# Kernel tuning notes

Measured on AMD Instinct MI355X. Metric: run time of the kernel, lower is better.

## Reference

```python
import jax, jax.numpy as jnp
import numpy as np


def pairwise_dist(x):
    # Euclidean cdist via the expansion trick; grad-safe sqrt (0 grad at 0, like torch).
    sq = jnp.sum(x * x, axis=1)
    d2 = sq[:, None] + sq[None, :] - 2.0 * (x @ x.T)
    d2 = jnp.maximum(d2, 0.0)
    pos = d2 > 0
    return jnp.where(pos, jnp.sqrt(jnp.where(pos, d2, 1.0)), 0.0)


def knn_mask(dist, k):
    # per-row ascending sort; skip index 0 (self), take next k neighbors
    idx = jnp.argsort(dist, axis=1)[:, 1:k + 1]            # [N, k]
    n = dist.shape[0]
    return jnp.zeros_like(dist).at[jnp.arange(n)[:, None], idx].set(1.0)


def setup_inputs() -> dict:
    key = jax.random.key(0)
    k1, k2 = jax.random.split(key)
    N, D, K = 8192, 64, 12
    latent = jax.random.normal(k1, (N, D), dtype=jnp.float32)
    latent_norm = jnp.ones((), dtype=jnp.float32)
    X = jax.random.normal(k2, (N, D), dtype=jnp.float32)
    dist_X = pairwise_dist(X)
    pair_mask_X = knn_mask(dist_X, K)
    return {"latent": latent, "latent_norm": latent_norm,
            "dist_X": dist_X, "pair_mask_X": pair_mask_X, "k": K}


def reference(latent, latent_norm, dist_X, pair_mask_X, k):
    n = latent.shape[0]
    dist_Z = pairwise_dist(latent) / latent_norm
    pair_mask_Z = knn_mask(dist_Z, k)

    mask_diff = pair_mask_Z - pair_mask_X
    matched = (n * k - jnp.sum(mask_diff != 0) * 0.5) / (n * k)

    # match_edges == 'symmetric'
    sig1 = dist_X * pair_mask_X
    sig1_2 = dist_Z * pair_mask_X
    distance1_2 = jnp.sum(jnp.square(sig1 - sig1_2))
    sig2 = dist_Z * pair_mask_Z
    sig2_1 = dist_X * pair_mask_Z
    distance2_1 = jnp.sum(jnp.square(sig2_1 - sig2))
    distance = distance1_2 + distance2_1
    return (distance, matched, distance1_2, distance2_1)
```

## Files before the change

### kernel.cpp

```cpp
#include <hip/hip_runtime.h>
#include <stdint.h>

constexpr int NPTS = 8192;
constexpr int DIM  = 64;
constexpr int KNN  = 12;

constexpr int RT = 64;
constexpr int CT = 64;
constexpr int CS = 4;
constexpr int STRIPE = NPTS / CS;
constexpr int NCHUNK = STRIPE / CT;
constexpr int LSTR = 72;

constexpr unsigned long long SENTINEL = 0xFFFFFFFFFFFFFFFFull;

typedef short bf16x8 __attribute__((ext_vector_type(8)));
typedef float f32x4  __attribute__((ext_vector_type(4)));

__device__ __forceinline__ unsigned short f2bf(float x) {
  unsigned u = __float_as_uint(x);
  return (unsigned short)((u + 0x7FFFu + ((u >> 16) & 1u)) >> 16);
}
__device__ __forceinline__ float bf2f(unsigned short h) {
  return __uint_as_float(((unsigned)h) << 16);
}

__global__ __launch_bounds__(256) void init_kernel(float* out, int* ecnt) {
  int g = blockIdx.x * 256 + threadIdx.x;
  if (g < NPTS) ecnt[g] = 0;
  if (g < 4) out[g] = 0.0f;
}

__global__ __launch_bounds__(256) void conv_kernel(
    const float* __restrict__ latent, unsigned short* __restrict__ Lh,
    unsigned short* __restrict__ Ll, float* __restrict__ sq) {
  int i = blockIdx.x * 256 + threadIdx.x;
  const float4* p = reinterpret_cast<const float4*>(latent + (size_t)i * DIM);
  float s = 0.f;
#pragma unroll
  for (int t = 0; t < DIM / 4; ++t) {
    float4 v = p[t];
    s += v.x * v.x + v.y * v.y + v.z * v.z + v.w * v.w;
    ushort4 h, l;
    h.x = f2bf(v.x); l.x = f2bf(v.x - bf2f(h.x));
    h.y = f2bf(v.y); l.y = f2bf(v.y - bf2f(h.y));
    h.z = f2bf(v.z); l.z = f2bf(v.z - bf2f(h.z));
    h.w = f2bf(v.w); l.w = f2bf(v.w - bf2f(h.w));
    *reinterpret_cast<ushort4*>(Lh + (size_t)i * DIM + t * 4) = h;
    *reinterpret_cast<ushort4*>(Ll + (size_t)i * DIM + t * 4) = l;
  }
  sq[i] = s;
}

__global__ __launch_bounds__(256) void scan_mask(
    const float* __restrict__ mask_X, const float* __restrict__ dist_X,
    int* __restrict__ ecnt, int* __restrict__ ecol, float* __restrict__ edx) {
  const int total4 = NPTS * NPTS / 4;
  int stride = gridDim.x * 256;
  for (int idx4 = blockIdx.x * 256 + threadIdx.x; idx4 < total4; idx4 += stride) {
    float4 m = reinterpret_cast<const float4*>(mask_X)[idx4];
    if (m.x == 0.f && m.y == 0.f && m.z == 0.f && m.w == 0.f) continue;
    int base = idx4 * 4;
    float mv[4] = {m.x, m.y, m.z, m.w};
#pragma unroll
    for (int c = 0; c < 4; ++c) {
      if (mv[c] != 0.f) {
        int pos = base + c;
        int i = pos >> 13, j = pos & (NPTS - 1);
        int slot = atomicAdd(&ecnt[i], 1);
        if (slot < KNN) {
          ecol[i * KNN + slot] = j;
          edx[i * KNN + slot] = dist_X[pos];
        }
      }
    }
  }
}

__device__ __forceinline__ void topk_insert(unsigned long long cand,
                                            unsigned long long pk[KNN]) {
#pragma unroll
  for (int s = KNN - 1; s >= 0; --s) {
    bool belongs = cand < pk[s];
    bool shift = (s > 0) && (cand < pk[s - 1]);
    unsigned long long nv = shift ? pk[s - 1] : cand;
    if (belongs) pk[s] = nv;
  }
}

__global__ __launch_bounds__(256, 2) void dz_main(
    const unsigned short* __restrict__ Lh, const unsigned short* __restrict__ Ll,
    const float* __restrict__ sq, unsigned long long* __restrict__ topk_ws) {
  __shared__ unsigned short Ah[RT * LSTR], Al[RT * LSTR];
  __shared__ unsigned short Bh[CT * LSTR], Bl[CT * LSTR];
  __shared__ unsigned long long buf[RT * CT];
  __shared__ int   cnt[RT];
  __shared__ float thr[RT];
  __shared__ float sqA[RT];
  __shared__ float sqB[CT];

  const int tid = threadIdx.x;
  const int tile = blockIdx.x / CS;
  const int split = blockIdx.x % CS;
  const int ib = tile * RT;
  const int jb0 = split * STRIPE;

  const int wid = tid >> 6;
  const int lane = tid & 63;
  const int quad = lane >> 4;
  const int l16 = lane & 15;
  const int wr = wid >> 1;
  const int wc = wid & 1;

#pragma unroll
  for (int it = 0; it < 2; ++it) {
    int f = it * 256 + tid;
    int r = f >> 3, c = f & 7;
    const uint4* sh = reinterpret_cast<const uint4*>(Lh + (size_t)(ib + r) * DIM + c * 8);
    const uint4* sl = reinterpret_cast<const uint4*>(Ll + (size_t)(ib + r) * DIM + c * 8);
    *reinterpret_cast<uint4*>(&Ah[r * LSTR + c * 8]) = *sh;
    *reinterpret_cast<uint4*>(&Al[r * LSTR + c * 8]) = *sl;
  }
  if (tid < RT) { sqA[tid] = sq[ib + tid]; thr[tid] = 3.4e38f; }

  unsigned long long pk[KNN];
#pragma unroll
  for (int t = 0; t < KNN; ++t) pk[t] = SENTINEL;

  for (int ch = 0; ch < NCHUNK; ++ch) {
    const int jb = jb0 + ch * CT;
    __syncthreads();
#pragma unroll
    for (int it = 0; it < 2; ++it) {
      int f = it * 256 + tid;
      int r = f >> 3, c = f & 7;
      const uint4* sh = reinterpret_cast<const uint4*>(Lh + (size_t)(jb + r) * DIM + c * 8);
      const uint4* sl = reinterpret_cast<const uint4*>(Ll + (size_t)(jb + r) * DIM + c * 8);
      *reinterpret_cast<uint4*>(&Bh[r * LSTR + c * 8]) = *sh;
      *reinterpret_cast<uint4*>(&Bl[r * LSTR + c * 8]) = *sl;
    }
    if (tid < CT) sqB[tid] = sq[jb + tid];
    if (tid < RT) cnt[tid] = 0;
    __syncthreads();

    f32x4 acc[2][2];
#pragma unroll
    for (int rb = 0; rb < 2; ++rb)
#pragma unroll
      for (int cb = 0; cb < 2; ++cb) acc[rb][cb] = (f32x4){0.f, 0.f, 0.f, 0.f};

#pragma unroll
    for (int kk = 0; kk < 2; ++kk) {
      const int ko = kk * 32 + quad * 8;
      bf16x8 ah[2], al[2], bh[2], bl[2];
#pragma unroll
      for (int rb = 0; rb < 2; ++rb) {
        int row = wr * 32 + rb * 16 + l16;
        ah[rb] = *reinterpret_cast<const bf16x8*>(&Ah[row * LSTR + ko]);
        al[rb] = *reinterpret_cast<const bf16x8*>(&Al[row * LSTR + ko]);
      }
#pragma unroll
      for (int cb = 0; cb < 2; ++cb) {
        int col = wc * 32 + cb * 16 + l16;
        bh[cb] = *reinterpret_cast<const bf16x8*>(&Bh[col * LSTR + ko]);
        bl[cb] = *reinterpret_cast<const bf16x8*>(&Bl[col * LSTR + ko]);
      }
#pragma unroll
      for (int rb = 0; rb < 2; ++rb)
#pragma unroll
        for (int cb = 0; cb < 2; ++cb) {
          acc[rb][cb] = __builtin_amdgcn_mfma_f32_16x16x32_bf16(ah[rb], bh[cb], acc[rb][cb], 0, 0, 0);
          acc[rb][cb] = __builtin_amdgcn_mfma_f32_16x16x32_bf16(ah[rb], bl[cb], acc[rb][cb], 0, 0, 0);
          acc[rb][cb] = __builtin_amdgcn_mfma_f32_16x16x32_bf16(al[rb], bh[cb], acc[rb][cb], 0, 0, 0);
        }
    }

#pragma unroll
    for (int rb = 0; rb < 2; ++rb) {
      const int row0 = wr * 32 + rb * 16 + quad * 4;
#pragma unroll
      for (int r = 0; r < 4; ++r) {
        const int rl = row0 + r;
        const int gi = ib + rl;
        const float sa = sqA[rl];
        const float t_thr = thr[rl];
#pragma unroll
        for (int cb = 0; cb < 2; ++cb) {
          const int col_l = wc * 32 + cb * 16 + l16;
          const int gj = jb + col_l;
          float d2 = sa + sqB[col_l] - 2.0f * acc[rb][cb][r];
          float d2c = fmaxf(d2, 0.0f);
          if (d2c < t_thr && gj != gi) {
            int pos = atomicAdd(&cnt[rl], 1);
            buf[rl * CT + pos] =
                ((unsigned long long)__float_as_uint(d2c) << 32) | (unsigned)gj;
          }
        }
      }
    }
    __syncthreads();

    if (tid < RT) {
      int n = cnt[tid];
      for (int t = 0; t < n; ++t) {
        unsigned long long cand = buf[tid * CT + t];
        if (cand < pk[KNN - 1]) topk_insert(cand, pk);
      }
      thr[tid] = __uint_as_float((unsigned)(pk[KNN - 1] >> 32));
    }
  }

  if (tid < RT) {
    size_t base = ((size_t)(ib + tid) * CS + split) * KNN;
#pragma unroll
    for (int t = 0; t < KNN; ++t) topk_ws[base + t] = pk[t];
  }
}

__global__ __launch_bounds__(256) void sig1_kernel(
    const float* __restrict__ latent, const float* __restrict__ latent_norm,
    const int* __restrict__ ecol, const float* __restrict__ edx,
    float* __restrict__ d_out) {
  __shared__ float red[256];
  const int tid = threadIdx.x;
  const int e = blockIdx.x * 256 + tid;
  const float invnorm = 1.0f / latent_norm[0];

  int i = e / KNN;
  int j = ecol[e];
  float dx = edx[e];
  const float4* a = reinterpret_cast<const float4*>(latent + (size_t)i * DIM);
  const float4* b = reinterpret_cast<const float4*>(latent + (size_t)j * DIM);
  float d2 = 0.f;
#pragma unroll
  for (int t = 0; t < DIM / 4; ++t) {
    float4 va = a[t], vb = b[t];
    float ex = va.x - vb.x, ey = va.y - vb.y, ez = va.z - vb.z, ew = va.w - vb.w;
    d2 += ex * ex + ey * ey + ez * ez + ew * ew;
  }
  float dz = (d2 > 0.f) ? sqrtf(d2) * invnorm : 0.f;
  float diff = dx - dz;
  float acc = diff * diff;

  red[tid] = acc;
  __syncthreads();
  for (int s = 128; s > 0; s >>= 1) {
    if (tid < s) red[tid] += red[tid + s];
    __syncthreads();
  }
  if (tid == 0) {
    atomicAdd(&d_out[2], red[0]);
    atomicAdd(&d_out[0], red[0]);
  }
}

__global__ __launch_bounds__(256) void finalize_kernel(
    const float* __restrict__ latent_norm, const float* __restrict__ dist_X,
    const int* __restrict__ ecol, const unsigned long long* __restrict__ topk_ws,
    float* __restrict__ d_out) {
  __shared__ float red[256];
  const int tid = threadIdx.x;
  const int gi = blockIdx.x * 256 + tid;
  const float invnorm = 1.0f / latent_norm[0];

  unsigned long long pk[KNN];
#pragma unroll
  for (int t = 0; t < KNN; ++t) pk[t] = SENTINEL;

  const unsigned long long* src = topk_ws + (size_t)gi * CS * KNN;
  for (int t = 0; t < CS * KNN; ++t) {
    unsigned long long cand = src[t];
    if (cand < pk[KNN - 1]) topk_insert(cand, pk);
  }

  int ec[KNN];
#pragma unroll
  for (int t = 0; t < KNN; ++t) ec[t] = ecol[gi * KNN + t];

  float acc2 = 0.f, accc = 0.f;
#pragma unroll
  for (int t = 0; t < KNN; ++t) {
    int j = (int)(unsigned)(pk[t] & 0xFFFFFFFFull);
    float d2 = __uint_as_float((unsigned)(pk[t] >> 32));
    float dz = (d2 > 0.0f) ? sqrtf(d2) * invnorm : 0.0f;
    float dxv = dist_X[(size_t)gi * NPTS + j];
    float diff = dxv - dz;
    acc2 += diff * diff;
    int hit = 0;
#pragma unroll
    for (int s = 0; s < KNN; ++s) hit |= (ec[s] == j);
    accc += (float)hit;
  }

  red[tid] = acc2;
  __syncthreads();
  for (int s = 128; s > 0; s >>= 1) {
    if (tid < s) red[tid] += red[tid + s];
    __syncthreads();
  }
  float racc2 = red[0];
  __syncthreads();
  red[tid] = accc;
  __syncthreads();
  for (int s = 128; s > 0; s >>= 1) {
    if (tid < s) red[tid] += red[tid + s];
    __syncthreads();
  }
  if (tid == 0) {
    atomicAdd(&d_out[3], racc2);
    atomicAdd(&d_out[0], racc2);
    atomicAdd(&d_out[1], red[0] * (1.0f / ((float)NPTS * (float)KNN)));
  }
}

extern "C" void kernel_launch(void* const* d_in, const int* in_sizes, int n_in,
                              void* d_out, int out_size, void* d_ws,
                              size_t ws_size, hipStream_t stream) {
  const float* latent      = (const float*)d_in[0];
  const float* latent_norm = (const float*)d_in[1];
  const float* dist_X      = (const float*)d_in[2];
  const float* mask_X      = (const float*)d_in[3];
  float* out = (float*)d_out;

  char* w = (char*)d_ws;
  float*          sq   = (float*)w;                    w += NPTS * 4;
  unsigned short* Lh   = (unsigned short*)w;           w += NPTS * DIM * 2;
  unsigned short* Ll   = (unsigned short*)w;           w += NPTS * DIM * 2;
  int*            ecnt = (int*)w;                      w += NPTS * 4;
  int*            ecol = (int*)w;                      w += NPTS * KNN * 4;
  float*          edx  = (float*)w;                    w += NPTS * KNN * 4;
  unsigned long long* topk = (unsigned long long*)w;

  init_kernel<<<NPTS / 256, 256, 0, stream>>>(out, ecnt);
  conv_kernel<<<NPTS / 256, 256, 0, stream>>>(latent, Lh, Ll, sq);
  scan_mask<<<2048, 256, 0, stream>>>(mask_X, dist_X, ecnt, ecol, edx);
  dz_main<<<(NPTS / RT) * CS, 256, 0, stream>>>(Lh, Ll, sq, topk);
  sig1_kernel<<<NPTS * KNN / 256, 256, 0, stream>>>(latent, latent_norm, ecol,
                                                    edx, out);
  finalize_kernel<<<NPTS / 256, 256, 0, stream>>>(latent_norm, dist_X, ecol,
                                                  topk, out);
}
```

Baseline: 663.4 us.

## Parallelize per-row top-k selection across all threads via score tile and merge

Replaces the per-chunk atomic candidate buffer, which only 64 threads drained serially, with a dense score tile in shared memory. Each of the 256 threads now keeps a private top-k over a 16-column slice of one row, and the four partial lists per row are merged at the end through a shared buffer that reuses the tile memory. The column split per row doubles, giving twice as many blocks, each with half the stripe. The trade is more insert work per thread, since the threshold-based pruning of candidates is gone, plus the final merge and an extra workspace pass.

```diff
diff --git a/kernel.cpp b/kernel.cpp
--- a/kernel.cpp
+++ b/kernel.cpp
@@ -7,10 +7,11 @@
 
 constexpr int RT = 64;
 constexpr int CT = 64;
-constexpr int CS = 4;
+constexpr int CS = 8;
 constexpr int STRIPE = NPTS / CS;
 constexpr int NCHUNK = STRIPE / CT;
 constexpr int LSTR = 72;
+constexpr int SSTR = 68;
 
 constexpr unsigned long long SENTINEL = 0xFFFFFFFFFFFFFFFFull;
 
@@ -91,13 +92,15 @@
 __global__ __launch_bounds__(256, 2) void dz_main(
     const unsigned short* __restrict__ Lh, const unsigned short* __restrict__ Ll,
     const float* __restrict__ sq, unsigned long long* __restrict__ topk_ws) {
-  __shared__ unsigned short Ah[RT * LSTR], Al[RT * LSTR];
-  __shared__ unsigned short Bh[CT * LSTR], Bl[CT * LSTR];
-  __shared__ unsigned long long buf[RT * CT];
-  __shared__ int   cnt[RT];
-  __shared__ float thr[RT];
-  __shared__ float sqA[RT];
-  __shared__ float sqB[CT];
+  __shared__ __align__(16) char smem[54784];
+  unsigned short* Ah = (unsigned short*)smem;
+  unsigned short* Al = Ah + RT * LSTR;
+  unsigned short* Bh = Al + RT * LSTR;
+  unsigned short* Bl = Bh + CT * LSTR;
+  float* Sc  = (float*)(smem + 4 * RT * LSTR * 2);
+  float* sqA = (float*)(smem + 4 * RT * LSTR * 2 + RT * SSTR * 4);
+  float* sqB = sqA + RT;
+  unsigned long long* mb = (unsigned long long*)smem;
 
   const int tid = threadIdx.x;
   const int tile = blockIdx.x / CS;
@@ -112,16 +115,19 @@
   const int wr = wid >> 1;
   const int wc = wid & 1;
 
+  const int srl = tid >> 2;
+  const int sqc = tid & 3;
+
 #pragma unroll
   for (int it = 0; it < 2; ++it) {
     int f = it * 256 + tid;
     int r = f >> 3, c = f & 7;
-    const uint4* sh = reinterpret_cast<const uint4*>(Lh + (size_t)(ib + r) * DIM + c * 8);
-    const uint4* sl = reinterpret_cast<const uint4*>(Ll + (size_t)(ib + r) * DIM + c * 8);
-    *reinterpret_cast<uint4*>(&Ah[r * LSTR + c * 8]) = *sh;
-    *reinterpret_cast<uint4*>(&Al[r * LSTR + c * 8]) = *sl;
-  }
-  if (tid < RT) { sqA[tid] = sq[ib + tid]; thr[tid] = 3.4e38f; }
+    *reinterpret_cast<uint4*>(&Ah[r * LSTR + c * 8]) =
+        *reinterpret_cast<const uint4*>(Lh + (size_t)(ib + r) * DIM + c * 8);
+    *reinterpret_cast<uint4*>(&Al[r * LSTR + c * 8]) =
+        *reinterpret_cast<const uint4*>(Ll + (size_t)(ib + r) * DIM + c * 8);
+  }
+  if (tid < RT) sqA[tid] = sq[ib + tid];
 
   unsigned long long pk[KNN];
 #pragma unroll
@@ -134,13 +140,12 @@
     for (int it = 0; it < 2; ++it) {
       int f = it * 256 + tid;
       int r = f >> 3, c = f & 7;
-      const uint4* sh = reinterpret_cast<const uint4*>(Lh + (size_t)(jb + r) * DIM + c * 8);
-      const uint4* sl = reinterpret_cast<const uint4*>(Ll + (size_t)(jb + r) * DIM + c * 8);
-      *reinterpret_cast<uint4*>(&Bh[r * LSTR + c * 8]) = *sh;
-      *reinterpret_cast<uint4*>(&Bl[r * LSTR + c * 8]) = *sl;
+      *reinterpret_cast<uint4*>(&Bh[r * LSTR + c * 8]) =
+          *reinterpret_cast<const uint4*>(Lh + (size_t)(jb + r) * DIM + c * 8);
+      *reinterpret_cast<uint4*>(&Bl[r * LSTR + c * 8]) =
+          *reinterpret_cast<const uint4*>(Ll + (size_t)(jb + r) * DIM + c * 8);
     }
     if (tid < CT) sqB[tid] = sq[jb + tid];
-    if (tid < RT) cnt[tid] = 0;
     __syncthreads();
 
     f32x4 acc[2][2];
@@ -181,39 +186,51 @@
 #pragma unroll
       for (int r = 0; r < 4; ++r) {
         const int rl = row0 + r;
+        const float sa = sqA[rl];
         const int gi = ib + rl;
-        const float sa = sqA[rl];
-        const float t_thr = thr[rl];
 #pragma unroll
         for (int cb = 0; cb < 2; ++cb) {
           const int col_l = wc * 32 + cb * 16 + l16;
           const int gj = jb + col_l;
           float d2 = sa + sqB[col_l] - 2.0f * acc[rb][cb][r];
           float d2c = fmaxf(d2, 0.0f);
-          if (d2c < t_thr && gj != gi) {
-            int pos = atomicAdd(&cnt[rl], 1);
-            buf[rl * CT + pos] =
-                ((unsigned long long)__float_as_uint(d2c) << 32) | (unsigned)gj;
-          }
+          Sc[rl * SSTR + col_l] = (gj == gi) ? 3.0e38f : d2c;
         }
       }
     }
     __syncthreads();
 
-    if (tid < RT) {
-      int n = cnt[tid];
-      for (int t = 0; t < n; ++t) {
-        unsigned long long cand = buf[tid * CT + t];
+    const int cbase = jb + sqc * 16;
+#pragma unroll
+    for (int s = 0; s < 16; s += 4) {
+      float4 v = *reinterpret_cast<const float4*>(&Sc[srl * SSTR + sqc * 16 + s]);
+      float va[4] = {v.x, v.y, v.z, v.w};
+#pragma unroll
+      for (int c = 0; c < 4; ++c) {
+        unsigned long long cand =
+            ((unsigned long long)__float_as_uint(va[c]) << 32) |
+            (unsigned)(cbase + s + c);
         if (cand < pk[KNN - 1]) topk_insert(cand, pk);
       }
-      thr[tid] = __uint_as_float((unsigned)(pk[KNN - 1] >> 32));
-    }
-  }
-
+    }
+  }
+
+  __syncthreads();
+#pragma unroll
+  for (int t = 0; t < KNN; ++t) mb[tid * KNN + t] = pk[t];
+  __syncthreads();
   if (tid < RT) {
+    unsigned long long fk[KNN];
+#pragma unroll
+    for (int t = 0; t < KNN; ++t) fk[t] = SENTINEL;
+    const unsigned long long* src = mb + tid * 4 * KNN;
+    for (int t = 0; t < 4 * KNN; ++t) {
+      unsigned long long cand = src[t];
+      if (cand < fk[KNN - 1]) topk_insert(cand, fk);
+    }
     size_t base = ((size_t)(ib + tid) * CS + split) * KNN;
 #pragma unroll
-    for (int t = 0; t < KNN; ++t) topk_ws[base + t] = pk[t];
+    for (int t = 0; t < KNN; ++t) topk_ws[base + t] = fk[t];
   }
 }
 
@@ -240,9 +257,8 @@
   }
   float dz = (d2 > 0.f) ? sqrtf(d2) * invnorm : 0.f;
   float diff = dx - dz;
-  float acc = diff * diff;
-
-  red[tid] = acc;
+
+  red[tid] = diff * diff;
   __syncthreads();
   for (int s = 128; s > 0; s >>= 1) {
     if (tid < s) red[tid] += red[tid + s];
```

After: 764.6 us. +15.2%, slower.
